# Optimization experiments

Measured on AMD Instinct MI355X. Metric: run time of the kernel, lower is better.

The kernel has to match this reference:

```python
import jax, jax.numpy as jnp
import numpy as np

B, N_T, D_A, D_V, D_U = 64, 8192, 2, 64, 1
L, MODES, X_PAD = 4, 64, 8


def setup_inputs() -> dict:
    key = jax.random.key(0)
    ks = jax.random.split(key, 9)
    scale = 1.0 / (D_V * D_V)  # Xavier-style gain used in original
    return {
        "v": jax.random.normal(ks[0], (B, N_T), dtype=jnp.float32),
        "grid": jax.random.uniform(ks[1], (N_T,), dtype=jnp.float32),
        "p_w": jax.random.normal(ks[2], (D_A, D_V), dtype=jnp.float32) * 0.1,
        "p_b": jnp.zeros((D_V,), dtype=jnp.float32),
        "fw": jax.random.normal(ks[3], (L, D_V, D_V, MODES, 2), dtype=jnp.float32) * scale,
        "w_w": jax.random.normal(ks[4], (L, D_V, D_V), dtype=jnp.float32) * (1.0 / np.sqrt(D_V)),
        "w_b": jnp.zeros((L, D_V), dtype=jnp.float32),
        "q_w": jax.random.normal(ks[5], (D_V, D_U), dtype=jnp.float32) * (1.0 / np.sqrt(D_V)),
        "q_b": jnp.zeros((D_U,), dtype=jnp.float32),
    }


def _fourier_layer(x, w):
    # x: (B, C, n), w: (C, C, modes, 2) real/imag channel-mixing weights
    n = x.shape[-1]
    xf = jnp.fft.rfft(x)                      # (B, C, n//2+1) complex
    xm = xf[:, :, :MODES]
    xr, xi = jnp.real(xm), jnp.imag(xm)
    wr, wi = w[..., 0], w[..., 1]
    out_r = jnp.einsum('bix,iox->box', xr, wr) - jnp.einsum('bix,iox->box', xi, wi)
    out_i = jnp.einsum('bix,iox->box', xi, wr) + jnp.einsum('bix,iox->box', xr, wi)
    out_m = jax.lax.complex(out_r, out_i)     # (B, C, modes)
    out_ft = jnp.pad(out_m, ((0, 0), (0, 0), (0, n // 2 + 1 - MODES)))
    return jnp.fft.irfft(out_ft, n=n)         # (B, C, n)


def reference(v, grid, p_w, p_b, fw, w_w, w_b, q_w, q_b):
    b, n = v.shape
    # lift: concat signal with coordinate channel -> (B, n, 2)
    x = jnp.concatenate([v[:, :, None], jnp.broadcast_to(grid[None, :, None], (b, n, 1))], axis=-1)
    x = x @ p_w + p_b                          # (B, n, d_v)
    x = jnp.transpose(x, (0, 2, 1))            # (B, d_v, n)
    x = jnp.pad(x, ((0, 0), (0, 0), (0, X_PAD)))
    for i in range(L):
        x1 = _fourier_layer(x, fw[i])
        x2 = jnp.einsum('bcn,cd->bdn', x, w_w[i]) + w_b[i][None, :, None]
        x = x1 + x2
        if i < L - 1:
            x = jax.nn.relu(x)
    x = x[..., :-X_PAD]                        # remove padding
    out = jnp.einsum('bcn,cd->bnd', x, q_w) + q_b  # (B, n, d_u)
    return out[..., 0]                         # d_u == 1 -> squeeze
```

## Files before the change

kernel.cpp:

```cpp
#include <hip/hip_runtime.h>

#define NT    8192
#define NP    8200
#define NPP   8320
#define NB    64
#define DV    64
#define NL    4
#define TFR   520
#define KSP   26
#define SPB   10
#define PI2   6.28318530717958647692f

typedef _Float16 half8 __attribute__((ext_vector_type(8)));
typedef _Float16 half4 __attribute__((ext_vector_type(4)));
typedef float    f32x4 __attribute__((ext_vector_type(4)));

static const size_t B_XT   = 0;
static const size_t B_TABF = 68157440ull;
static const size_t B_TABI = B_TABF + 2129920ull;
static const size_t B_WFR  = B_TABI + 2129920ull;
static const size_t B_ZFR  = B_WFR  + 131072ull;
static const size_t B_XPF  = B_ZFR  + 1048576ull;
static const size_t B_VP   = B_XPF  + 27262976ull;
static const size_t B_G    = B_VP   + 425984ull;
static const size_t B_A    = B_G    + 512ull;

__global__ void k_prep(_Float16* __restrict__ tabF, _Float16* __restrict__ tabI) {
    int idx = blockIdx.x * 256 + threadIdx.x;
    if (idx < 133120) {
        int lane = idx & 63;
        int rest = idx >> 6;
        int cf = rest & 7, gs = rest >> 3;
        int ml = lane & 15, lh = lane >> 4;
        int m = cf * 16 + ml, k = m >> 1, comp = m & 1;
        half8 o;
        #pragma unroll
        for (int j = 0; j < 8; ++j) {
            int t = gs * 32 + lh * 8 + j;
            float val = 0.f;
            if (t < NP) {
                int mm = (int)(((long long)t * (long long)k) % NP);
                float th = (float)mm * (PI2 / (float)NP);
                float sn, cs; sincosf(th, &sn, &cs);
                val = comp ? sn : cs;
            }
            o[j] = (_Float16)val;
        }
        *(half8*)&tabF[(size_t)idx * 8] = o;
    } else if (idx < 266240) {
        int id2 = idx - 133120;
        int lane = id2 & 63;
        int rest = id2 >> 6;
        int tf = rest % 520, ks = rest / 520;
        int lt = lane & 15, mh = lane >> 4;
        int t = tf * 16 + lt;
        half8 o;
        #pragma unroll
        for (int j = 0; j < 8; ++j) {
            int m = ks * 32 + mh * 8 + j;
            int k = m >> 1, comp = m & 1;
            float val = 0.f;
            if (t < NP) {
                int mm = (int)(((long long)t * (long long)k) % NP);
                float th = (float)mm * (PI2 / (float)NP);
                float sn, cs; sincosf(th, &sn, &cs);
                float al = (k == 0) ? (1.f / NP) : (2.f / NP);
                val = al * (comp ? sn : cs);
            }
            o[j] = (_Float16)val;
        }
        *(half8*)&tabI[(size_t)id2 * 8] = o;
    }
}

__global__ void k_prep_w(const float* __restrict__ ww, _Float16* __restrict__ Wfrag) {
    int idx = blockIdx.x * 256 + threadIdx.x;
    if (idx >= NL * DV * DV) return;
    int l = idx >> 12, cd = idx & 4095, c = cd >> 6, d = cd & 63;
    float wv = ww[((size_t)l * DV + c) * DV + d];
    _Float16 h = (_Float16)wv;
    _Float16 lo = (_Float16)(wv - (float)h);
    int ks = c >> 5, mf = d >> 4;
    int lane = (d & 15) + 16 * ((c >> 3) & 3), j = c & 7;
    Wfrag[((((size_t)l * 2 + 0) * 2 + ks) * 4 + mf) * 512 + (size_t)lane * 8 + j] = h;
    Wfrag[((((size_t)l * 2 + 1) * 2 + ks) * 4 + mf) * 512 + (size_t)lane * 8 + j] = lo;
}

__global__ void k_prep_p(const float* __restrict__ pw, const float* __restrict__ pb,
                         const float* __restrict__ ww, float* __restrict__ A) {
    int d = threadIdx.x;
    float a0 = 0.f, a1 = 0.f, a2 = 0.f;
    #pragma unroll 8
    for (int c = 0; c < DV; ++c) {
        float w = ww[(size_t)c * DV + d];
        a0 = fmaf(pw[c], w, a0);
        a1 = fmaf(pw[DV + c], w, a1);
        a2 = fmaf(pb[c], w, a2);
    }
    A[d] = a0; A[64 + d] = a1; A[128 + d] = a2;
}

__global__ void k_gd(const float* __restrict__ grd, float* __restrict__ G) {
    __shared__ float rb[256];
    int m = blockIdx.x, k = m >> 1, comp = m & 1;
    int tid = threadIdx.x;
    float s = 0.f;
    for (int t = tid; t < NT; t += 256) {
        int mm = (int)(((long long)t * (long long)k) % NP);
        float th = (float)mm * (PI2 / (float)NP);
        float sn, cs; sincosf(th, &sn, &cs);
        s += grd[t] * (comp ? sn : cs);
    }
    rb[tid] = s; __syncthreads();
    for (int h = 128; h > 0; h >>= 1) { if (tid < h) rb[tid] += rb[tid + h]; __syncthreads(); }
    if (tid == 0) G[m] = rb[0];
}

__launch_bounds__(256)
__global__ void k_fdft_v(const float* __restrict__ v, const _Float16* __restrict__ tabF,
                         _Float16* __restrict__ Vp) {
    int ksb = blockIdx.x;
    int tid = threadIdx.x, w = tid >> 6, lane = tid & 63, g = lane >> 4, r = lane & 15;
    const half8* tFv = (const half8*)tabF;
    f32x4 acc[4][2];
    #pragma unroll
    for (int mf = 0; mf < 4; ++mf)
        #pragma unroll
        for (int nf = 0; nf < 2; ++nf) acc[mf][nf] = (f32x4){0.f, 0.f, 0.f, 0.f};
    for (int s = 0; s < SPB; ++s) {
        int gs = ksb * SPB + s;
        int t0 = gs * 32 + g * 8;
        half8 a[4];
        #pragma unroll
        for (int mf = 0; mf < 4; ++mf) {
            int brow = mf * 16 + r;
            half8 hv;
            if (t0 < NT) {
                const float4* pv = (const float4*)&v[(size_t)brow * NT + t0];
                float4 v0 = pv[0], v1 = pv[1];
                hv[0] = (_Float16)v0.x; hv[1] = (_Float16)v0.y; hv[2] = (_Float16)v0.z; hv[3] = (_Float16)v0.w;
                hv[4] = (_Float16)v1.x; hv[5] = (_Float16)v1.y; hv[6] = (_Float16)v1.z; hv[7] = (_Float16)v1.w;
            } else {
                #pragma unroll
                for (int j = 0; j < 8; ++j) hv[j] = (_Float16)0.f;
            }
            a[mf] = hv;
        }
        half8 bb[2];
        #pragma unroll
        for (int nf = 0; nf < 2; ++nf) bb[nf] = tFv[((size_t)gs * 8 + w * 2 + nf) * 64 + lane];
        #pragma unroll
        for (int mf = 0; mf < 4; ++mf)
            #pragma unroll
            for (int nf = 0; nf < 2; ++nf)
                acc[mf][nf] = __builtin_amdgcn_mfma_f32_16x16x32_f16(a[mf], bb[nf], acc[mf][nf], 0, 0, 0);
    }
    #pragma unroll
    for (int mf = 0; mf < 4; ++mf)
        #pragma unroll
        for (int nf = 0; nf < 2; ++nf)
            #pragma unroll
            for (int reg = 0; reg < 4; ++reg) {
                int brow = mf * 16 + g * 4 + reg;
                int m = w * 32 + nf * 16 + r;
                Vp[((size_t)ksb * NB + brow) * 128 + m] = (_Float16)acc[mf][nf][reg];
            }
}

__launch_bounds__(256)
__global__ void k_fdft(const _Float16* __restrict__ xT, const _Float16* __restrict__ tabF,
                       _Float16* __restrict__ xpf) {
    __shared__ _Float16 xls[2][2048];
    int sb = blockIdx.x, b = blockIdx.y;
    int tid = threadIdx.x, w = tid >> 6, lane = tid & 63, g = lane >> 4, r = lane & 15;
    const half8* tFv = (const half8*)tabF;
    f32x4 acc[4][2];
    #pragma unroll
    for (int cf = 0; cf < 4; ++cf)
        #pragma unroll
        for (int nf = 0; nf < 2; ++nf) acc[cf][nf] = (f32x4){0.f, 0.f, 0.f, 0.f};
    int tl = tid >> 3, c0 = (tid & 7) * 8;

    half8 vv = *(const half8*)&xT[((size_t)b * NPP + (sb * SPB) * 32 + tl) * 64 + c0];
    #pragma unroll
    for (int j = 0; j < 8; ++j) {
        int c = c0 + j;
        xls[0][c * 32 + (tl ^ (((c >> 3) & 3) << 3))] = vv[j];
    }
    int cur = 0;
    #pragma unroll 1
    for (int s = 0; s < SPB; ++s) {
        int gs = sb * SPB + s;
        half8 vvn;
        if (s + 1 < SPB)
            vvn = *(const half8*)&xT[((size_t)b * NPP + (gs + 1) * 32 + tl) * 64 + c0];
        __syncthreads();
        if (s + 1 < SPB) {
            #pragma unroll
            for (int j = 0; j < 8; ++j) {
                int c = c0 + j;
                xls[cur ^ 1][c * 32 + (tl ^ (((c >> 3) & 3) << 3))] = vvn[j];
            }
        }
        half8 a[4], bb[2];
        #pragma unroll
        for (int cf = 0; cf < 4; ++cf) {
            int c = cf * 16 + r;
            a[cf] = *(const half8*)&xls[cur][c * 32 + ((g * 8) ^ ((((c >> 3) & 3)) << 3))];
        }
        #pragma unroll
        for (int nf = 0; nf < 2; ++nf) bb[nf] = tFv[((size_t)gs * 8 + w * 2 + nf) * 64 + lane];
        #pragma unroll
        for (int cf = 0; cf < 4; ++cf)
            #pragma unroll
            for (int nf = 0; nf < 2; ++nf)
                acc[cf][nf] = __builtin_amdgcn_mfma_f32_16x16x32_f16(a[cf], bb[nf], acc[cf][nf], 0, 0, 0);
        cur ^= 1;
    }
    _Float16* xp = xpf + (((size_t)sb * NB + b) * 4 + w) * 2048;
    #pragma unroll
    for (int cf = 0; cf < 4; ++cf)
        #pragma unroll
        for (int nf = 0; nf < 2; ++nf) {
            half4 h4;
            #pragma unroll
            for (int reg = 0; reg < 4; ++reg) h4[reg] = (_Float16)acc[cf][nf][reg];
            *(half4*)&xp[(cf * 2 + nf) * 256 + lane * 4] = h4;
        }
}

__launch_bounds__(256)
__global__ void k_spec0(const _Float16* __restrict__ Vp, const float* __restrict__ G,
                        const float* __restrict__ pw, const float* __restrict__ pb,
                        const float* __restrict__ fw_l, _Float16* __restrict__ zfr) {
    __shared__ float Xs[64][32];
    __shared__ float Vs[32], Gs[32];
    int b = blockIdx.y, kq = blockIdx.x, tid = threadIdx.x;
    if (tid < 32) {
        int m = kq * 32 + tid;
        float ssum = 0.f;
        #pragma unroll
        for (int ks = 0; ks < KSP; ++ks) ssum += (float)Vp[((size_t)ks * NB + b) * 128 + m];
        Vs[tid] = ssum;
        Gs[tid] = G[m];
    }
    __syncthreads();
    #pragma unroll
    for (int q = 0; q < 8; ++q) {
        int flat = q * 256 + tid;
        int i = flat >> 5, ml = flat & 31;
        float xv = pw[i] * Vs[ml] + pw[64 + i] * Gs[ml];
        if (kq == 0 && ml == 0) xv += pb[i] * (float)NT;
        Xs[i][ml] = xv;
    }
    __syncthreads();
    #pragma unroll
    for (int q = 0; q < 4; ++q) {
        int flat = q * 256 + tid;
        int o = flat >> 4, kl = flat & 15;
        int k = kq * 16 + kl;
        float yr = 0.f, yi = 0.f;
        #pragma unroll 8
        for (int i = 0; i < 64; ++i) {
            float2 xv = *(const float2*)&Xs[i][2 * kl];
            float2 wv = *(const float2*)&fw_l[(((size_t)i * DV + o) * 64 + k) * 2];
            yr = fmaf(xv.x, wv.x, fmaf(xv.y, wv.y, yr));
            yi = fmaf(xv.x, wv.y, fmaf(-xv.y, wv.x, yi));
        }
        int mf = o >> 4, mm = 2 * kl, m1 = mm + 1;
        zfr[((((size_t)b * 4 + kq) * 4 + mf) * 64 + (o & 15) + 16 * (mm >> 3)) * 8 + (mm & 7)] = (_Float16)yr;
        zfr[((((size_t)b * 4 + kq) * 4 + mf) * 64 + (o & 15) + 16 * (m1 >> 3)) * 8 + (m1 & 7)] = (_Float16)(-yi);
    }
}

__launch_bounds__(256)
__global__ void k_spec(const _Float16* __restrict__ xpf, const float* __restrict__ fw_l,
                       _Float16* __restrict__ zfr) {
    __shared__ float Xs[64][32];
    int b = blockIdx.y, kq = blockIdx.x, tid = threadIdx.x;
    float a8[8];
    #pragma unroll
    for (int e = 0; e < 8; ++e) a8[e] = 0.f;
    const half8* src = (const half8*)xpf;
    size_t base8 = ((size_t)b * 4 + kq) * 256 + tid;
    const size_t step8 = (size_t)NB * 4 * 256;
    for (int ks = 0; ks < KSP; ++ks) {
        half8 vv = src[base8 + (size_t)ks * step8];
        #pragma unroll
        for (int e = 0; e < 8; ++e) a8[e] += (float)vv[e];
    }
    int cf = tid >> 6, nf2 = (tid >> 5) & 1, lane0 = (tid & 31) * 2;
    #pragma unroll
    for (int e = 0; e < 8; ++e) {
        int lane = lane0 + (e >> 2), reg = e & 3;
        int g = lane >> 4, r = lane & 15;
        Xs[cf * 16 + g * 4 + reg][nf2 * 16 + r] = a8[e];
    }
    __syncthreads();
    #pragma unroll
    for (int q = 0; q < 4; ++q) {
        int flat = q * 256 + tid;
        int o = flat >> 4, kl = flat & 15;
        int k = kq * 16 + kl;
        float yr = 0.f, yi = 0.f;
        #pragma unroll 8
        for (int i = 0; i < 64; ++i) {
            float2 xv = *(const float2*)&Xs[i][2 * kl];
            float2 wv = *(const float2*)&fw_l[(((size_t)i * DV + o) * 64 + k) * 2];
            yr = fmaf(xv.x, wv.x, fmaf(xv.y, wv.y, yr));
            yi = fmaf(xv.x, wv.y, fmaf(-xv.y, wv.x, yi));
        }
        int mf = o >> 4, mm = 2 * kl, m1 = mm + 1;
        zfr[((((size_t)b * 4 + kq) * 4 + mf) * 64 + (o & 15) + 16 * (mm >> 3)) * 8 + (mm & 7)] = (_Float16)yr;
        zfr[((((size_t)b * 4 + kq) * 4 + mf) * 64 + (o & 15) + 16 * (m1 >> 3)) * 8 + (m1 & 7)] = (_Float16)(-yi);
    }
}

template <int MODE>
__launch_bounds__(128)
__global__ void k_inv(const _Float16* __restrict__ zfr, const _Float16* __restrict__ tabI,
                      const _Float16* __restrict__ Wl, const float* __restrict__ wb_l,
                      const float* __restrict__ qw, const float* __restrict__ qb,
                      const float* __restrict__ v, const float* __restrict__ grd,
                      const float* __restrict__ A,
                      _Float16* __restrict__ xT, float* __restrict__ out) {
    __shared__ _Float16 xw[2][2048];
    __shared__ float Asm[3][64];
    int b = blockIdx.y;
    int tid = threadIdx.x, w = tid >> 6, lane = tid & 63;
    int wid = blockIdx.x * 2 + w;
    int g = lane >> 4, r = lane & 15;
    int tw = wid * 32;
    const half8* zfv = (const half8*)zfr;
    const half8* tIv = (const half8*)tabI;
    const half8* wfv = (const half8*)Wl;

    if (MODE == 0) {
        Asm[0][lane] = A[lane];
        Asm[1][lane] = A[64 + lane];
        Asm[2][lane] = A[128 + lane];
    }

    f32x4 acc[4][2];
    #pragma unroll
    for (int mf = 0; mf < 4; ++mf)
        #pragma unroll
        for (int nf = 0; nf < 2; ++nf) acc[mf][nf] = (f32x4){0.f, 0.f, 0.f, 0.f};

    #pragma unroll
    for (int ks4 = 0; ks4 < 4; ++ks4) {
        half8 az[4], bt[2];
        #pragma unroll
        for (int mf = 0; mf < 4; ++mf)
            az[mf] = zfv[(((size_t)b * 4 + ks4) * 4 + mf) * 64 + lane];
        #pragma unroll
        for (int nf = 0; nf < 2; ++nf)
            bt[nf] = tIv[((size_t)ks4 * TFR + (tw >> 4) + nf) * 64 + lane];
        #pragma unroll
        for (int mf = 0; mf < 4; ++mf)
            #pragma unroll
            for (int nf = 0; nf < 2; ++nf)
                acc[mf][nf] = __builtin_amdgcn_mfma_f32_16x16x32_f16(az[mf], bt[nf], acc[mf][nf], 0, 0, 0);
    }
    if (MODE != 0) {
        half8 xb[2][2];
        #pragma unroll
        for (int ks = 0; ks < 2; ++ks)
            #pragma unroll
            for (int nf = 0; nf < 2; ++nf)
                xb[ks][nf] = *(const half8*)&xT[((size_t)b * NPP + tw + nf * 16 + r) * 64 + ks * 32 + g * 8];
        #pragma unroll
        for (int hl = 0; hl < 2; ++hl)
            #pragma unroll
            for (int ks = 0; ks < 2; ++ks) {
                half8 aw[4];
                #pragma unroll
                for (int mf = 0; mf < 4; ++mf)
                    aw[mf] = wfv[((size_t)(hl * 2 + ks) * 4 + mf) * 64 + lane];
                #pragma unroll
                for (int mf = 0; mf < 4; ++mf)
                    #pragma unroll
                    for (int nf = 0; nf < 2; ++nf)
                        acc[mf][nf] = __builtin_amdgcn_mfma_f32_16x16x32_f16(aw[mf], xb[ks][nf], acc[mf][nf], 0, 0, 0);
            }
    }

    if (MODE != 2) {
        float vv[2], gg[2];
        if (MODE == 0) {
            #pragma unroll
            for (int nf = 0; nf < 2; ++nf) {
                int t = tw + nf * 16 + r;
                bool in = (t < NT);
                vv[nf] = in ? v[(size_t)b * NT + t] : 0.f;
                gg[nf] = in ? grd[t] : 0.f;
            }
        }
        #pragma unroll
        for (int mf = 0; mf < 4; ++mf)
            #pragma unroll
            for (int nf = 0; nf < 2; ++nf) {
                int tl = nf * 16 + r;
                half4 h4;
                #pragma unroll
                for (int reg = 0; reg < 4; ++reg) {
                    int o = mf * 16 + g * 4 + reg;
                    float val = acc[mf][nf][reg] + wb_l[o];
                    if (MODE == 0)
                        val += fmaf(Asm[0][o], vv[nf], fmaf(Asm[1][o], gg[nf], Asm[2][o]));
                    h4[reg] = (_Float16)fmaxf(val, 0.f);
                }
                int idx = tl * 64 + ((mf * 16 + g * 4) ^ ((tl & 7) << 3));
                *(half4*)&xw[w][idx] = h4;
            }
        #pragma unroll
        for (int it = 0; it < 4; ++it) {
            int t = it * 8 + (lane >> 3);
            int cg = lane & 7;
            half8 vv8 = *(const half8*)&xw[w][t * 64 + ((cg * 8) ^ ((t & 7) << 3))];
            *(half8*)&xT[((size_t)b * NPP + tw + t) * 64 + cg * 8] = vv8;
        }
    } else {
        float p0 = 0.f, p1 = 0.f;
        #pragma unroll
        for (int mf = 0; mf < 4; ++mf)
            #pragma unroll
            for (int reg = 0; reg < 4; ++reg) {
                int o = mf * 16 + g * 4 + reg;
                float qq = qw[o], bias = wb_l[o];
                p0 = fmaf(acc[mf][0][reg] + bias, qq, p0);
                p1 = fmaf(acc[mf][1][reg] + bias, qq, p1);
            }
        p0 += __shfl_xor(p0, 16); p0 += __shfl_xor(p0, 32);
        p1 += __shfl_xor(p1, 16); p1 += __shfl_xor(p1, 32);
        float qbv = qb[0];
        if (g == 0) out[(size_t)b * NT + tw + r]      = p0 + qbv;
        if (g == 1) out[(size_t)b * NT + tw + 16 + r] = p1 + qbv;
    }
}

extern "C" void kernel_launch(void* const* d_in, const int* in_sizes, int n_in,
                              void* d_out, int out_size, void* d_ws, size_t ws_size,
                              hipStream_t stream) {
    const float* v   = (const float*)d_in[0];
    const float* grd = (const float*)d_in[1];
    const float* pw  = (const float*)d_in[2];
    const float* pb  = (const float*)d_in[3];
    const float* fw  = (const float*)d_in[4];
    const float* ww  = (const float*)d_in[5];
    const float* wb  = (const float*)d_in[6];
    const float* qw  = (const float*)d_in[7];
    const float* qb  = (const float*)d_in[8];
    float* out = (float*)d_out;

    char* wsb = (char*)d_ws;
    _Float16* xT    = (_Float16*)(wsb + B_XT);
    _Float16* tabFb = (_Float16*)(wsb + B_TABF);
    _Float16* tabIb = (_Float16*)(wsb + B_TABI);
    _Float16* Wfrag = (_Float16*)(wsb + B_WFR);
    _Float16* zfrag = (_Float16*)(wsb + B_ZFR);
    _Float16* xpf   = (_Float16*)(wsb + B_XPF);
    _Float16* Vpart = (_Float16*)(wsb + B_VP);
    float*    G     = (float*)(wsb + B_G);
    float*    A     = (float*)(wsb + B_A);

    k_prep<<<1040, 256, 0, stream>>>(tabFb, tabIb);
    k_prep_w<<<(NL * DV * DV + 255) / 256, 256, 0, stream>>>(ww, Wfrag);
    k_prep_p<<<1, 64, 0, stream>>>(pw, pb, ww, A);
    k_gd<<<128, 256, 0, stream>>>(grd, G);
    k_fdft_v<<<KSP, 256, 0, stream>>>(v, tabFb, Vpart);

    for (int l = 0; l < NL; ++l) {
        if (l == 0) {
            k_spec0<<<dim3(4, NB), 256, 0, stream>>>(Vpart, G, pw, pb, fw, zfrag);
        } else {
            k_fdft<<<dim3(KSP, NB), 256, 0, stream>>>(xT, tabFb, xpf);
            k_spec<<<dim3(4, NB), 256, 0, stream>>>(xpf, fw + (size_t)l * DV * DV * 64 * 2, zfrag);
        }
        const _Float16* wf_l = Wfrag + (size_t)l * 8192;
        const float* wb_l = wb + (size_t)l * DV;
        if (l == 0)
            k_inv<0><<<dim3(130, NB), 128, 0, stream>>>(
                zfrag, tabIb, wf_l, wb_l, qw, qb, v, grd, A, xT, out);
        else if (l < NL - 1)
            k_inv<1><<<dim3(130, NB), 128, 0, stream>>>(
                zfrag, tabIb, wf_l, wb_l, qw, qb, v, grd, A, xT, out);
        else
            k_inv<2><<<dim3(128, NB), 128, 0, stream>>>(
                zfrag, tabIb, wf_l, wb_l, qw, qb, v, grd, A, xT, out);
    }
}
```

Measured before the change: 305.1 us.

## Fuse forward DFT of next layer into inverse-DFT kernel epilogue

Removes the separate k_fdft kernel. Each k_inv block now covers 128 time points with 256 threads, keeps its post-ReLU activations in shared memory, and computes the partial forward DFT for the next layer directly from that shared tile. The cost targeted is the reread of xT and the extra launch per layer. In exchange there are more partial sums (65 instead of 26), which enlarges xpf and the reduction work in k_spec. It also adds a syncthreads and a larger shared buffer that may lower occupancy. k_inv<2> still runs the fused DFT needlessly unless MODE gating excludes it, and xT is still written.

```diff
diff --git a/kernel.cpp b/kernel.cpp
--- a/kernel.cpp
+++ b/kernel.cpp
@@ -7,8 +7,9 @@
 #define DV    64
 #define NL    4
 #define TFR   520
-#define KSP   26
-#define SPB   10
+#define KSP   65
+#define KSPV  26
+#define SPBV  10
 #define PI2   6.28318530717958647692f
 
 typedef _Float16 half8 __attribute__((ext_vector_type(8)));
@@ -21,7 +22,7 @@
 static const size_t B_WFR  = B_TABI + 2129920ull;
 static const size_t B_ZFR  = B_WFR  + 131072ull;
 static const size_t B_XPF  = B_ZFR  + 1048576ull;
-static const size_t B_VP   = B_XPF  + 27262976ull;
+static const size_t B_VP   = B_XPF  + 68157440ull;
 static const size_t B_G    = B_VP   + 425984ull;
 static const size_t B_A    = B_G    + 512ull;
 
@@ -127,8 +128,8 @@
     for (int mf = 0; mf < 4; ++mf)
         #pragma unroll
         for (int nf = 0; nf < 2; ++nf) acc[mf][nf] = (f32x4){0.f, 0.f, 0.f, 0.f};
-    for (int s = 0; s < SPB; ++s) {
-        int gs = ksb * SPB + s;
+    for (int s = 0; s < SPBV; ++s) {
+        int gs = ksb * SPBV + s;
         int t0 = gs * 32 + g * 8;
         half8 a[4];
         #pragma unroll
@@ -165,68 +166,6 @@
                 int m = w * 32 + nf * 16 + r;
                 Vp[((size_t)ksb * NB + brow) * 128 + m] = (_Float16)acc[mf][nf][reg];
             }
-}
-
-__launch_bounds__(256)
-__global__ void k_fdft(const _Float16* __restrict__ xT, const _Float16* __restrict__ tabF,
-                       _Float16* __restrict__ xpf) {
-    __shared__ _Float16 xls[2][2048];
-    int sb = blockIdx.x, b = blockIdx.y;
-    int tid = threadIdx.x, w = tid >> 6, lane = tid & 63, g = lane >> 4, r = lane & 15;
-    const half8* tFv = (const half8*)tabF;
-    f32x4 acc[4][2];
-    #pragma unroll
-    for (int cf = 0; cf < 4; ++cf)
-        #pragma unroll
-        for (int nf = 0; nf < 2; ++nf) acc[cf][nf] = (f32x4){0.f, 0.f, 0.f, 0.f};
-    int tl = tid >> 3, c0 = (tid & 7) * 8;
-
-    half8 vv = *(const half8*)&xT[((size_t)b * NPP + (sb * SPB) * 32 + tl) * 64 + c0];
-    #pragma unroll
-    for (int j = 0; j < 8; ++j) {
-        int c = c0 + j;
-        xls[0][c * 32 + (tl ^ (((c >> 3) & 3) << 3))] = vv[j];
-    }
-    int cur = 0;
-    #pragma unroll 1
-    for (int s = 0; s < SPB; ++s) {
-        int gs = sb * SPB + s;
-        half8 vvn;
-        if (s + 1 < SPB)
-            vvn = *(const half8*)&xT[((size_t)b * NPP + (gs + 1) * 32 + tl) * 64 + c0];
-        __syncthreads();
-        if (s + 1 < SPB) {
-            #pragma unroll
-            for (int j = 0; j < 8; ++j) {
-                int c = c0 + j;
-                xls[cur ^ 1][c * 32 + (tl ^ (((c >> 3) & 3) << 3))] = vvn[j];
-            }
-        }
-        half8 a[4], bb[2];
-        #pragma unroll
-        for (int cf = 0; cf < 4; ++cf) {
-            int c = cf * 16 + r;
-            a[cf] = *(const half8*)&xls[cur][c * 32 + ((g * 8) ^ ((((c >> 3) & 3)) << 3))];
-        }
-        #pragma unroll
-        for (int nf = 0; nf < 2; ++nf) bb[nf] = tFv[((size_t)gs * 8 + w * 2 + nf) * 64 + lane];
-        #pragma unroll
-        for (int cf = 0; cf < 4; ++cf)
-            #pragma unroll
-            for (int nf = 0; nf < 2; ++nf)
-                acc[cf][nf] = __builtin_amdgcn_mfma_f32_16x16x32_f16(a[cf], bb[nf], acc[cf][nf], 0, 0, 0);
-        cur ^= 1;
-    }
-    _Float16* xp = xpf + (((size_t)sb * NB + b) * 4 + w) * 2048;
-    #pragma unroll
-    for (int cf = 0; cf < 4; ++cf)
-        #pragma unroll
-        for (int nf = 0; nf < 2; ++nf) {
-            half4 h4;
-            #pragma unroll
-            for (int reg = 0; reg < 4; ++reg) h4[reg] = (_Float16)acc[cf][nf][reg];
-            *(half4*)&xp[(cf * 2 + nf) * 256 + lane * 4] = h4;
-        }
 }
 
 __launch_bounds__(256)
@@ -240,7 +179,7 @@
         int m = kq * 32 + tid;
         float ssum = 0.f;
         #pragma unroll
-        for (int ks = 0; ks < KSP; ++ks) ssum += (float)Vp[((size_t)ks * NB + b) * 128 + m];
+        for (int ks = 0; ks < KSPV; ++ks) ssum += (float)Vp[((size_t)ks * NB + b) * 128 + m];
         Vs[tid] = ssum;
         Gs[tid] = G[m];
     }
@@ -317,22 +256,23 @@
 }
 
 template <int MODE>
-__launch_bounds__(128)
+__launch_bounds__(256)
 __global__ void k_inv(const _Float16* __restrict__ zfr, const _Float16* __restrict__ tabI,
-                      const _Float16* __restrict__ Wl, const float* __restrict__ wb_l,
-                      const float* __restrict__ qw, const float* __restrict__ qb,
-                      const float* __restrict__ v, const float* __restrict__ grd,
-                      const float* __restrict__ A,
-                      _Float16* __restrict__ xT, float* __restrict__ out) {
-    __shared__ _Float16 xw[2][2048];
+                      const _Float16* __restrict__ tabF, const _Float16* __restrict__ Wl,
+                      const float* __restrict__ wb_l, const float* __restrict__ qw,
+                      const float* __restrict__ qb, const float* __restrict__ v,
+                      const float* __restrict__ grd, const float* __restrict__ A,
+                      _Float16* __restrict__ xT, _Float16* __restrict__ xpf,
+                      float* __restrict__ out) {
+    __shared__ _Float16 xc[64 * 128];
     __shared__ float Asm[3][64];
-    int b = blockIdx.y;
+    int b = blockIdx.y, bx = blockIdx.x;
     int tid = threadIdx.x, w = tid >> 6, lane = tid & 63;
-    int wid = blockIdx.x * 2 + w;
     int g = lane >> 4, r = lane & 15;
-    int tw = wid * 32;
+    int tw = bx * 128 + w * 32;
     const half8* zfv = (const half8*)zfr;
     const half8* tIv = (const half8*)tabI;
+    const half8* tFv = (const half8*)tabF;
     const half8* wfv = (const half8*)Wl;
 
     if (MODE == 0) {
@@ -400,26 +340,63 @@
         for (int mf = 0; mf < 4; ++mf)
             #pragma unroll
             for (int nf = 0; nf < 2; ++nf) {
-                int tl = nf * 16 + r;
-                half4 h4;
+                int tb = w * 32 + nf * 16 + r;
                 #pragma unroll
                 for (int reg = 0; reg < 4; ++reg) {
                     int o = mf * 16 + g * 4 + reg;
                     float val = acc[mf][nf][reg] + wb_l[o];
                     if (MODE == 0)
                         val += fmaf(Asm[0][o], vv[nf], fmaf(Asm[1][o], gg[nf], Asm[2][o]));
-                    h4[reg] = (_Float16)fmaxf(val, 0.f);
+                    xc[o * 128 + (tb ^ (((o >> 2) & 3) << 3))] = (_Float16)fmaxf(val, 0.f);
                 }
-                int idx = tl * 64 + ((mf * 16 + g * 4) ^ ((tl & 7) << 3));
-                *(half4*)&xw[w][idx] = h4;
             }
         #pragma unroll
         for (int it = 0; it < 4; ++it) {
-            int t = it * 8 + (lane >> 3);
-            int cg = lane & 7;
-            half8 vv8 = *(const half8*)&xw[w][t * 64 + ((cg * 8) ^ ((t & 7) << 3))];
-            *(half8*)&xT[((size_t)b * NPP + tw + t) * 64 + cg * 8] = vv8;
-        }
+            int tl = it * 8 + (lane >> 3);
+            int tb = w * 32 + tl;
+            int c0 = (lane & 7) * 8;
+            half8 vv8;
+            #pragma unroll
+            for (int jj = 0; jj < 8; ++jj) {
+                int c = c0 + jj;
+                vv8[jj] = xc[c * 128 + (tb ^ (((c >> 2) & 3) << 3))];
+            }
+            *(half8*)&xT[((size_t)b * NPP + tw + tl) * 64 + c0] = vv8;
+        }
+        __syncthreads();
+        f32x4 dacc[4][2];
+        #pragma unroll
+        for (int cf = 0; cf < 4; ++cf)
+            #pragma unroll
+            for (int nf = 0; nf < 2; ++nf) dacc[cf][nf] = (f32x4){0.f, 0.f, 0.f, 0.f};
+        #pragma unroll
+        for (int step = 0; step < 4; ++step) {
+            int gs = bx * 4 + step;
+            half8 a[4], bb[2];
+            #pragma unroll
+            for (int cf = 0; cf < 4; ++cf) {
+                int c = cf * 16 + r;
+                a[cf] = *(const half8*)&xc[c * 128 + ((step * 32 + g * 8) ^ (((c >> 2) & 3) << 3))];
+            }
+            #pragma unroll
+            for (int nf = 0; nf < 2; ++nf)
+                bb[nf] = tFv[((size_t)gs * 8 + w * 2 + nf) * 64 + lane];
+            #pragma unroll
+            for (int cf = 0; cf < 4; ++cf)
+                #pragma unroll
+                for (int nf = 0; nf < 2; ++nf)
+                    dacc[cf][nf] = __builtin_amdgcn_mfma_f32_16x16x32_f16(a[cf], bb[nf], dacc[cf][nf], 0, 0, 0);
+        }
+        _Float16* xp = xpf + (((size_t)bx * NB + b) * 4 + w) * 2048;
+        #pragma unroll
+        for (int cf = 0; cf < 4; ++cf)
+            #pragma unroll
+            for (int nf = 0; nf < 2; ++nf) {
+                half4 h4;
+                #pragma unroll
+                for (int reg = 0; reg < 4; ++reg) h4[reg] = (_Float16)dacc[cf][nf][reg];
+                *(half4*)&xp[(cf * 2 + nf) * 256 + lane * 4] = h4;
+            }
     } else {
         float p0 = 0.f, p1 = 0.f;
         #pragma unroll
@@ -468,25 +445,23 @@
     k_prep_w<<<(NL * DV * DV + 255) / 256, 256, 0, stream>>>(ww, Wfrag);
     k_prep_p<<<1, 64, 0, stream>>>(pw, pb, ww, A);
     k_gd<<<128, 256, 0, stream>>>(grd, G);
-    k_fdft_v<<<KSP, 256, 0, stream>>>(v, tabFb, Vpart);
+    k_fdft_v<<<KSPV, 256, 0, stream>>>(v, tabFb, Vpart);
 
     for (int l = 0; l < NL; ++l) {
-        if (l == 0) {
+        if (l == 0)
             k_spec0<<<dim3(4, NB), 256, 0, stream>>>(Vpart, G, pw, pb, fw, zfrag);
-        } else {
-            k_fdft<<<dim3(KSP, NB), 256, 0, stream>>>(xT, tabFb, xpf);
+        else
             k_spec<<<dim3(4, NB), 256, 0, stream>>>(xpf, fw + (size_t)l * DV * DV * 64 * 2, zfrag);
-        }
         const _Float16* wf_l = Wfrag + (size_t)l * 8192;
         const float* wb_l = wb + (size_t)l * DV;
         if (l == 0)
-            k_inv<0><<<dim3(130, NB), 128, 0, stream>>>(
-                zfrag, tabIb, wf_l, wb_l, qw, qb, v, grd, A, xT, out);
+            k_inv<0><<<dim3(65, NB), 256, 0, stream>>>(
+                zfrag, tabIb, tabFb, wf_l, wb_l, qw, qb, v, grd, A, xT, xpf, out);
         else if (l < NL - 1)
-            k_inv<1><<<dim3(130, NB), 128, 0, stream>>>(
-                zfrag, tabIb, wf_l, wb_l, qw, qb, v, grd, A, xT, out);
+            k_inv<1><<<dim3(65, NB), 256, 0, stream>>>(
+                zfrag, tabIb, tabFb, wf_l, wb_l, qw, qb, v, grd, A, xT, xpf, out);
         else
-            k_inv<2><<<dim3(128, NB), 128, 0, stream>>>(
-                zfrag, tabIb, wf_l, wb_l, qw, qb, v, grd, A, xT, out);
-    }
-}
+            k_inv<2><<<dim3(64, NB), 256, 0, stream>>>(
+                zfrag, tabIb, tabFb, wf_l, wb_l, qw, qb, v, grd, A, xT, xpf, out);
+    }
+}
```

New measurement: 344.2 us. +12.8%, slower.
